# Optimization experiments

Measured on AMD Instinct MI355X. Metric: run time of the kernel, lower is better.

Reference implementation:

```python
import jax, jax.numpy as jnp
import numpy as np

# Hyperparameters (from init_kwargs)
D_MODEL = 1024
D_STATE = 64
HEADDIM = 64
MIMO_RANK = 2
CHUNK = 128
EXPAND = 2
D_INNER = EXPAND * D_MODEL            # 2048
NHEADS = D_INNER // HEADDIM           # 32
G = MIMO_RANK * D_STATE               # effective state channels per head = 128
D_CONV = 4
D_XBC = D_INNER + 2 * NHEADS * G      # conv channels
D_IN_PROJ = 2 * D_INNER + 2 * NHEADS * G + NHEADS  # [z, x, B, C, dt]


def rmsnorm(x, w, eps=1e-5):
    return x * w * jax.lax.rsqrt(jnp.mean(x * x, axis=-1, keepdims=True) + eps)


def setup_inputs() -> dict:
    key = jax.random.key(0)
    ks = jax.random.split(key, 8)
    B, L = 2, 2048
    x = jax.random.normal(ks[0], (B, L, D_MODEL), jnp.float32)
    norm_w = jnp.ones((D_MODEL,), jnp.float32)
    in_proj_w = jax.random.normal(ks[1], (D_IN_PROJ, D_MODEL), jnp.float32) * 0.02
    conv_w = jax.random.normal(ks[2], (D_XBC, D_CONV), jnp.float32) * 0.2
    conv_b = jnp.zeros((D_XBC,), jnp.float32)
    dt_bias = jax.random.uniform(ks[3], (NHEADS,), jnp.float32, minval=-4.0, maxval=-1.0)
    A_log = jnp.log(jax.random.uniform(ks[4], (NHEADS,), jnp.float32, minval=1.0, maxval=8.0))
    D_skip = jnp.ones((NHEADS,), jnp.float32)
    gnorm_w = jnp.ones((D_INNER,), jnp.float32)
    out_proj_w = jax.random.normal(ks[5], (D_MODEL, D_INNER), jnp.float32) * 0.02
    return dict(x=x, norm_w=norm_w, in_proj_w=in_proj_w, conv_w=conv_w, conv_b=conv_b,
                dt_bias=dt_bias, A_log=A_log, D_skip=D_skip, gnorm_w=gnorm_w,
                out_proj_w=out_proj_w)


def _mamba3(u, in_proj_w, conv_w, conv_b, dt_bias, A_log, D_skip, gnorm_w, out_proj_w):
    B, L, _ = u.shape
    H, P = NHEADS, HEADDIM
    nc = L // CHUNK

    zxbcdt = u @ in_proj_w.T                                   # (B,L,D_IN_PROJ)
    z, xbc, dt_raw = jnp.split(zxbcdt, [D_INNER, D_INNER + D_XBC], axis=-1)

    # causal depthwise conv (width D_CONV) + SiLU on [x, B, C]
    xp = jnp.pad(xbc, ((0, 0), (D_CONV - 1, 0), (0, 0)))
    conv = conv_b + sum(xp[:, k:k + L, :] * conv_w[:, k] for k in range(D_CONV))
    xbc = jax.nn.silu(conv)
    xh, Bm, Cm = jnp.split(xbc, [D_INNER, D_INNER + H * G], axis=-1)

    Xc = xh.reshape(B, nc, CHUNK, H, P)
    Bc = Bm.reshape(B, nc, CHUNK, H, G)
    Cc = Cm.reshape(B, nc, CHUNK, H, G)

    dt = jax.nn.softplus(dt_raw + dt_bias)                     # (B,L,H), positive
    A = -jnp.exp(A_log)                                        # (H,), negative
    dtc = dt.reshape(B, nc, CHUNK, H)
    a = dtc * A                                                # log decay, (B,nc,cs,H)
    cum = jnp.cumsum(a, axis=2)                                # inclusive cumsum within chunk

    # intra-chunk (quadratic, causal) part
    cumT = cum.transpose(0, 1, 3, 2)                           # (B,nc,H,cs)
    diff = cumT[..., :, None] - cumT[..., None, :]             # cum_l - cum_s
    mask = jnp.tril(jnp.ones((CHUNK, CHUNK), bool))
    decay = jnp.where(mask, jnp.exp(jnp.where(mask, diff, 0.0)), 0.0)
    dtT = dtc.transpose(0, 1, 3, 2)                            # (B,nc,H,cs)
    scores = jnp.einsum('bclhg,bcshg->bchls', Cc, Bc) * decay * dtT[:, :, :, None, :]
    Y_intra = jnp.einsum('bchls,bcshp->bclhp', scores, Xc)

    # inter-chunk state recurrence
    w = jnp.exp(cum[:, :, -1:, :] - cum) * dtc                 # (B,nc,cs,H)
    S = jnp.einsum('bcshg,bcshp->bchgp', Bc * w[..., None], Xc)  # chunk states
    dlast = jnp.exp(cum[:, :, -1, :])                          # (B,nc,H) total chunk decay

    def step(carry, inp):
        dl, s = inp
        return dl[:, :, None, None] * carry + s, carry

    init = jnp.zeros((B, H, G, P), u.dtype)
    _, Hprev = jax.lax.scan(step, init, (dlast.transpose(1, 0, 2), S.transpose(1, 0, 2, 3, 4)))
    Hprev = Hprev.transpose(1, 0, 2, 3, 4)                     # (B,nc,H,G,P) state before chunk
    Y_inter = jnp.einsum('bclhg,bchgp->bclhp', Cc * jnp.exp(cum)[..., None], Hprev)

    y = (Y_intra + Y_inter + D_skip[:, None] * Xc).reshape(B, L, D_INNER)
    y = rmsnorm(y * jax.nn.silu(z), gnorm_w)                   # gated RMSNorm
    return y @ out_proj_w.T


def reference(x, norm_w, in_proj_w, conv_w, conv_b, dt_bias, A_log, D_skip, gnorm_w, out_proj_w):
    # pre-norm residual wrapper
    return x + _mamba3(rmsnorm(x, norm_w), in_proj_w, conv_w, conv_b,
                       dt_bias, A_log, D_skip, gnorm_w, out_proj_w)
```

## Files before the change

### kernel.cpp

```cpp
#include <hip/hip_runtime.h>

typedef unsigned short u16;
typedef __attribute__((ext_vector_type(8))) short bf16x8;
typedef __attribute__((ext_vector_type(4))) float f32x4;

#define MFMA16(a,b,c) __builtin_amdgcn_mfma_f32_16x16x32_bf16(a,b,c,0,0,0)

#define DMODEL   1024
#define DINNER   2048
#define NHEADS   32
#define HEADDIM  64
#define GDIM     128
#define DXBC     10240
#define DPROJ    12320
#define CHUNK_L  128
#define NCHUNK   16
#define NROWS    4096

__device__ __forceinline__ float b2f(u16 u){ return __uint_as_float(((unsigned)u)<<16); }
__device__ __forceinline__ u16 f2b(float f){
  unsigned u = __float_as_uint(f);
  u += 0x7fffu + ((u>>16)&1u);
  return (u16)(u>>16);
}

__device__ __forceinline__ void gload_lds16(const void* g, void* l){
  __builtin_amdgcn_global_load_lds(
      (const __attribute__((address_space(1))) unsigned int*)g,
      (__attribute__((address_space(3))) unsigned int*)l, 16, 0, 0);
}

__global__ void k_f32_to_bf16(const float* __restrict__ src, u16* __restrict__ dst, int n){
  int i = blockIdx.x*blockDim.x + threadIdx.x;
  int stride = gridDim.x*blockDim.x;
  int n4 = n >> 2;
  for (int j=i; j<n4; j+=stride){
    float4 v = reinterpret_cast<const float4*>(src)[j];
    uint2 o;
    o.x = (unsigned)f2b(v.x) | ((unsigned)f2b(v.y)<<16);
    o.y = (unsigned)f2b(v.z) | ((unsigned)f2b(v.w)<<16);
    reinterpret_cast<uint2*>(dst)[j] = o;
  }
}

__global__ __launch_bounds__(256) void k_rmsnorm_in(const float* __restrict__ x,
                                                    const float* __restrict__ w,
                                                    u16* __restrict__ u){
  int row = blockIdx.x, tid = threadIdx.x;
  float4 v = reinterpret_cast<const float4*>(x + (size_t)row*DMODEL)[tid];
  float ss = v.x*v.x + v.y*v.y + v.z*v.z + v.w*v.w;
  #pragma unroll
  for (int off=32; off>0; off>>=1) ss += __shfl_down(ss, off, 64);
  __shared__ float red[4];
  if ((tid&63)==0) red[tid>>6] = ss;
  __syncthreads();
  float tot = red[0]+red[1]+red[2]+red[3];
  float sc = rsqrtf(tot/(float)DMODEL + 1e-5f);
  float4 wv = reinterpret_cast<const float4*>(w)[tid];
  uint2 o;
  o.x = (unsigned)f2b(v.x*wv.x*sc) | ((unsigned)f2b(v.y*wv.y*sc)<<16);
  o.y = (unsigned)f2b(v.z*wv.z*sc) | ((unsigned)f2b(v.w*wv.w*sc)<<16);
  reinterpret_cast<uint2*>(u + (size_t)row*DMODEL)[tid] = o;
}

__global__ __launch_bounds__(512) void k_gemm1_8ph(const u16* __restrict__ A,
                                                   const u16* __restrict__ W,
                                                   u16* __restrict__ zb,
                                                   u16* __restrict__ xbc){
  __shared__ __align__(16) u16 lds[4*16384];
  const int tid  = threadIdx.x;
  const int lane = tid & 63, w = tid >> 6;
  const int wr = w >> 2, wc = w & 3;
  int bid = blockIdx.x;
  int xcd = bid & 7, g = bid >> 3;
  int st  = xcd*6 + (g >> 4);
  int wi  = g & 15;
  int tm  = (st/12)*4 + (wi>>2);
  int tn  = (st%12)*4 + (wi&3);
  const int m0 = tm*256, n0 = tn*256;

  const int srcslot = ((lane&3) ^ ((lane>>3)&3)) * 8;
  const u16* aS0 = A + (size_t)(m0 + w*16 + (lane>>2))*DMODEL + srcslot;
  const u16* aS1 = aS0 + (size_t)128*DMODEL;
  const u16* bS0 = W + (size_t)(n0 + w*16 + (lane>>2))*DMODEL + srcslot;
  const u16* bS1 = bS0 + (size_t)128*DMODEL;
  const int ldsW = (w*16)*32;
  const int rr = lane & 15;
  const int kb = (((lane>>4) ^ ((lane>>1)&3))) * 8;

  f32x4 acc[8][4];
  #pragma unroll
  for (int i=0;i<8;i++)
    #pragma unroll
    for (int j=0;j<4;j++) acc[i][j] = (f32x4){0,0,0,0};

  int stage_off = 0;
  auto STAGE = [&](int slot){
    u16* base = lds + slot*16384;
    gload_lds16(aS0 + stage_off, base + ldsW);
    gload_lds16(aS1 + stage_off, base + 128*32 + ldsW);
    gload_lds16(bS0 + stage_off, base + 8192 + ldsW);
    gload_lds16(bS1 + stage_off, base + 8192 + 128*32 + ldsW);
    stage_off += 32;
  };
  auto KTILE = [&](int kt, bool do_stage){
    int slot = kt & 3;
    if (do_stage) STAGE((kt+3)&3);
    const u16* As = lds + slot*16384;
    const u16* Bs = As + 8192;
    bf16x8 bf[4];
    #pragma unroll
    for (int tj=0;tj<4;tj++)
      bf[tj] = *(const bf16x8*)&Bs[(wc*64 + tj*16 + rr)*32 + kb];
    #pragma unroll
    for (int r=0;r<2;r++){
      bf16x8 af[4];
      #pragma unroll
      for (int ti=0;ti<4;ti++)
        af[ti] = *(const bf16x8*)&As[(wr*128 + r*64 + ti*16 + rr)*32 + kb];
      __builtin_amdgcn_s_setprio(1);
      #pragma unroll
      for (int ti=0;ti<4;ti++)
        #pragma unroll
        for (int tj=0;tj<4;tj++)
          acc[r*4+ti][tj] = MFMA16(af[ti], bf[tj], acc[r*4+ti][tj]);
      __builtin_amdgcn_s_setprio(0);
    }
  };

  STAGE(0); STAGE(1); STAGE(2);
  asm volatile("s_waitcnt vmcnt(8)" ::: "memory");
  __builtin_amdgcn_s_barrier();
  __builtin_amdgcn_sched_barrier(0);

  for (int kt = 0; kt < 29; ++kt){
    KTILE(kt, true);
    asm volatile("s_waitcnt vmcnt(8)" ::: "memory");
    __builtin_amdgcn_s_barrier();
    __builtin_amdgcn_sched_barrier(0);
  }
  KTILE(29, false);
  asm volatile("s_waitcnt vmcnt(4)" ::: "memory");
  __builtin_amdgcn_s_barrier();
  __builtin_amdgcn_sched_barrier(0);
  KTILE(30, false);
  asm volatile("s_waitcnt vmcnt(0)" ::: "memory");
  __builtin_amdgcn_s_barrier();
  __builtin_amdgcn_sched_barrier(0);
  KTILE(31, false);

  const int row0 = m0 + wr*128 + (lane>>4)*4;
  const int colb = wc*64 + (lane&15);
  if (tn >= 8){
    const int cb = n0 - DINNER;
    #pragma unroll
    for (int ti=0;ti<8;ti++)
      #pragma unroll
      for (int tj=0;tj<4;tj++)
        #pragma unroll
        for (int q=0;q<4;q++)
          xbc[(size_t)(row0 + ti*16 + q)*DXBC + cb + colb + tj*16] = f2b(acc[ti][tj][q]);
  } else {
    #pragma unroll
    for (int ti=0;ti<8;ti++)
      #pragma unroll
      for (int tj=0;tj<4;tj++)
        #pragma unroll
        for (int q=0;q<4;q++)
          zb[(size_t)(row0 + ti*16 + q)*DINNER + n0 + colb + tj*16] = f2b(acc[ti][tj][q]);
  }
}

template<int K>
__device__ __forceinline__ void gemm_core(const u16* __restrict__ A, const u16* __restrict__ W,
                                          int m0, int n0, u16* As, u16* Bs, f32x4 acc[4][4]){
  const int tid  = threadIdx.x;
  const int lane = tid & 63, wv = tid >> 6;
  const int wr = wv >> 1, wc = wv & 1;
  const int r4 = lane >> 2, c8 = (lane & 3) * 8;
  const int rr = lane & 15, kb = (lane >> 4) * 8;

  const u16* aS = A + (size_t)(m0 + wv*32 + r4)*K + c8;
  const u16* bS = W + (size_t)(n0 + wv*32 + r4)*K + c8;
  u16* aD = As + (wv*32)*32;
  u16* bD = Bs + (wv*32)*32;

  #pragma unroll
  for (int i=0;i<4;i++)
    #pragma unroll
    for (int j=0;j<4;j++) acc[i][j] = (f32x4){0,0,0,0};

  for (int k0 = 0; k0 < K; k0 += 32){
    gload_lds16(aS + k0,        aD);
    gload_lds16(aS + 16*K + k0, aD + 16*32);
    gload_lds16(bS + k0,        bD);
    gload_lds16(bS + 16*K + k0, bD + 16*32);
    asm volatile("s_waitcnt vmcnt(0)");
    __syncthreads();
    bf16x8 af[4], bw[4];
    #pragma unroll
    for (int t=0;t<4;t++){
      af[t] = *(const bf16x8*)&As[(wr*64 + t*16 + rr)*32 + kb];
      bw[t] = *(const bf16x8*)&Bs[(wc*64 + t*16 + rr)*32 + kb];
    }
    #pragma unroll
    for (int ti=0;ti<4;ti++)
      #pragma unroll
      for (int tj=0;tj<4;tj++)
        acc[ti][tj] = MFMA16(af[ti], bw[tj], acc[ti][tj]);
    __syncthreads();
  }
}

__global__ __launch_bounds__(256) void k_gemm_dt(const u16* __restrict__ A,
                                                 const u16* __restrict__ W,
                                                 float* __restrict__ dtraw){
  const int lane = threadIdx.x & 63, wv = threadIdx.x >> 6;
  const int m0 = blockIdx.x*32;
  const int n0 = DINNER + DXBC;
  const int r  = lane & 15;
  const int kb = (lane>>4)*8;
  const int k0 = wv*256;
  const u16* a0p = A + (size_t)(m0 + r)*DMODEL + k0 + kb;
  const u16* a1p = a0p + 16*DMODEL;
  const u16* b0p = W + (size_t)(n0 + r)*DMODEL + k0 + kb;
  const u16* b1p = b0p + 16*DMODEL;
  f32x4 acc00={0,0,0,0}, acc01={0,0,0,0}, acc10={0,0,0,0}, acc11={0,0,0,0};
  #pragma unroll
  for (int k=0;k<256;k+=32){
    bf16x8 a0 = *(const bf16x8*)(a0p + k);
    bf16x8 a1 = *(const bf16x8*)(a1p + k);
    bf16x8 b0 = *(const bf16x8*)(b0p + k);
    bf16x8 b1 = *(const bf16x8*)(b1p + k);
    acc00 = MFMA16(a0,b0,acc00);
    acc01 = MFMA16(a0,b1,acc01);
    acc10 = MFMA16(a1,b0,acc10);
    acc11 = MFMA16(a1,b1,acc11);
  }
  __shared__ float part[4][1024];
  int rowb = (lane>>4)*4, col = lane&15;
  #pragma unroll
  for (int rr=0; rr<4; rr++){
    part[wv][(rowb+rr)*32 + col]         = acc00[rr];
    part[wv][(rowb+rr)*32 + col+16]      = acc01[rr];
    part[wv][(rowb+16+rr)*32 + col]      = acc10[rr];
    part[wv][(rowb+16+rr)*32 + col+16]   = acc11[rr];
  }
  __syncthreads();
  int idx = threadIdx.x*4;
  #pragma unroll
  for (int q=0;q<4;q++){
    int i = idx+q;
    dtraw[(size_t)m0*NHEADS + i] = part[0][i]+part[1][i]+part[2][i]+part[3][i];
  }
}

__global__ __launch_bounds__(256) void k_conv(const u16* __restrict__ xbc,
                                              const float* __restrict__ cw,
                                              const float* __restrict__ cb,
                                              u16* __restrict__ xh,
                                              u16* __restrict__ Bm,
                                              u16* __restrict__ Cm){
  int c  = (blockIdx.x*256 + threadIdx.x)*2;
  int row0 = blockIdx.y*8;
  int l0 = row0 & 2047;
  float4 wa = reinterpret_cast<const float4*>(cw)[c];
  float4 wb = reinterpret_cast<const float4*>(cw)[c+1];
  float cba = cb[c], cbb = cb[c+1];
  float a3=0,a2=0,a1=0, b3=0,b2=0,b1=0;
  auto loadpair = [&](int rw, float& fa, float& fb){
    unsigned v = *(const unsigned*)&xbc[(size_t)rw*DXBC + c];
    fa = b2f((u16)v); fb = b2f((u16)(v>>16));
  };
  if (l0 >= 3){
    loadpair(row0-3, a3,b3); loadpair(row0-2, a2,b2); loadpair(row0-1, a1,b1);
  }
  #pragma unroll
  for (int i=0;i<8;i++){
    float a0,b0; loadpair(row0+i, a0,b0);
    float sa = cba + a3*wa.x + a2*wa.y + a1*wa.z + a0*wa.w;
    float sb = cbb + b3*wb.x + b2*wb.y + b1*wb.z + b0*wb.w;
    sa = sa/(1.f+expf(-sa)); sb = sb/(1.f+expf(-sb));
    unsigned o = (unsigned)f2b(sa) | ((unsigned)f2b(sb)<<16);
    int rw = row0 + i;
    if (c < DINNER)            *(unsigned*)&xh[(size_t)rw*DINNER + c] = o;
    else if (c < DINNER+4096)  *(unsigned*)&Bm[(size_t)rw*4096 + (c-DINNER)] = o;
    else                       *(unsigned*)&Cm[(size_t)rw*4096 + (c-DINNER-4096)] = o;
    a3=a2; a2=a1; a1=a0; b3=b2; b2=b1; b1=b0;
  }
}

__global__ __launch_bounds__(128) void k_dtscan(const float* __restrict__ dtraw,
                                                const float* __restrict__ dt_bias,
                                                const float* __restrict__ A_log,
                                                float* __restrict__ dtT,
                                                float* __restrict__ cumT){
  int blk = blockIdx.x;
  int h   = blk & 31;
  int bc  = blk >> 5;
  int s   = threadIdx.x;
  int row = bc*128 + s;
  float xv = dtraw[(size_t)row*NHEADS + h] + dt_bias[h];
  float dt = (xv > 20.f) ? xv : log1pf(expf(xv));
  float a  = dt * (-expf(A_log[h]));
  __shared__ float lds[128];
  lds[s] = a; __syncthreads();
  #pragma unroll
  for (int off=1; off<128; off<<=1){
    float t = (s>=off) ? lds[s-off] : 0.f;
    __syncthreads();
    lds[s] += t;
    __syncthreads();
  }
  dtT[(size_t)blk*128 + s]  = dt;
  cumT[(size_t)blk*128 + s] = lds[s];
}

__global__ __launch_bounds__(256) void k_states(const u16* __restrict__ Bm,
                                                const u16* __restrict__ xh,
                                                const float* __restrict__ dtT,
                                                const float* __restrict__ cumT,
                                                float* __restrict__ S){
  int blk = blockIdx.x;
  int h = blk & 31, bc = blk >> 5;
  __shared__ __align__(16) u16 Bw[128][136];
  __shared__ __align__(16) u16 XT[64][136];
  __shared__ float cum[128], dtv[128];
  int tid = threadIdx.x;
  if (tid < 128){ cum[tid] = cumT[(size_t)blk*128+tid]; dtv[tid] = dtT[(size_t)blk*128+tid]; }
  __syncthreads();
  float clast = cum[127];
  for (int i = tid; i < 128*128; i += 256){
    int s = i >> 7, g = i & 127;
    float w = expf(clast - cum[s]) * dtv[s];
    Bw[g][s] = f2b(b2f(Bm[(size_t)(bc*128+s)*4096 + h*128 + g]) * w);
  }
  for (int i = tid; i < 64*128; i += 256){
    int s = i >> 6, p = i & 63;
    XT[p][s] = xh[(size_t)(bc*128+s)*DINNER + h*64 + p];
  }
  __syncthreads();
  int lane = tid & 63, wv = tid >> 6;
  int r = lane & 15, kb = (lane>>4)*8;
  f32x4 acc[2][4];
  #pragma unroll
  for (int i=0;i<2;i++)
    #pragma unroll
    for (int j=0;j<4;j++) acc[i][j] = (f32x4){0,0,0,0};
  #pragma unroll
  for (int k=0;k<128;k+=32){
    bf16x8 a0 = *(const bf16x8*)&Bw[wv*32 + r][k+kb];
    bf16x8 a1 = *(const bf16x8*)&Bw[wv*32 + 16 + r][k+kb];
    #pragma unroll
    for (int tj=0;tj<4;tj++){
      bf16x8 bb = *(const bf16x8*)&XT[tj*16 + r][k+kb];
      acc[0][tj] = MFMA16(a0,bb,acc[0][tj]);
      acc[1][tj] = MFMA16(a1,bb,acc[1][tj]);
    }
  }
  float* Sp = S + (size_t)blk*8192;
  int g0 = wv*32 + (lane>>4)*4, p0 = lane&15;
  #pragma unroll
  for (int ti=0;ti<2;ti++)
    #pragma unroll
    for (int tj=0;tj<4;tj++)
      #pragma unroll
      for (int rr=0;rr<4;rr++)
        Sp[(g0 + ti*16 + rr)*64 + tj*16 + p0] = acc[ti][tj][rr];
}

__global__ __launch_bounds__(256) void k_scan(const float* __restrict__ S,
                                              const float* __restrict__ cumT,
                                              u16* __restrict__ Hp){
  int slice = blockIdx.x & 7;
  int bh = blockIdx.x >> 3;
  int b = bh >> 5, h = bh & 31;
  int e0 = slice*1024 + threadIdx.x*4;
  float4 carry = {0,0,0,0};
  for (int c=0;c<NCHUNK;c++){
    int blk = (b*16+c)*32 + h;
    float dl = expf(cumT[(size_t)blk*128 + 127]);
    float4 s = *(const float4*)&S[(size_t)blk*8192 + e0];
    uint2 o;
    o.x = (unsigned)f2b(carry.x) | ((unsigned)f2b(carry.y)<<16);
    o.y = (unsigned)f2b(carry.z) | ((unsigned)f2b(carry.w)<<16);
    *reinterpret_cast<uint2*>(&Hp[(size_t)blk*8192 + e0]) = o;
    carry.x = dl*carry.x + s.x;
    carry.y = dl*carry.y + s.y;
    carry.z = dl*carry.z + s.z;
    carry.w = dl*carry.w + s.w;
  }
}

__global__ __launch_bounds__(256) void k_intra(const u16* __restrict__ Cm,
                                               const u16* __restrict__ Bm,
                                               const u16* __restrict__ xh,
                                               const u16* __restrict__ Hp,
                                               const float* __restrict__ dtT,
                                               const float* __restrict__ cumT,
                                               const float* __restrict__ Dskip,
                                               u16* __restrict__ yh){
  int blk = blockIdx.x;
  int h = blk & 31, bc = blk >> 5;
  __shared__ __align__(16) u16 Cl[128][136];
  __shared__ __align__(16) u16 Bl[128][136];
  __shared__ __align__(16) u16 XT[64][136];
  __shared__ __align__(16) u16 HT[64][136];
  __shared__ float cum[128], dtv[128];
  int tid = threadIdx.x;
  if (tid < 128){ cum[tid] = cumT[(size_t)blk*128+tid]; dtv[tid] = dtT[(size_t)blk*128+tid]; }
  for (int i = tid; i < 128*128; i += 256){
    int rw = i >> 7, g = i & 127;
    Cl[rw][g] = Cm[(size_t)(bc*128+rw)*4096 + h*128 + g];
    Bl[rw][g] = Bm[(size_t)(bc*128+rw)*4096 + h*128 + g];
  }
  for (int i = tid; i < 64*128; i += 256){
    int s = i >> 6, p = i & 63;
    XT[p][s] = xh[(size_t)(bc*128+s)*DINNER + h*64 + p];
  }
  for (int i = tid; i < 64*128; i += 256){
    int g = i >> 6, p = i & 63;
    HT[p][g] = Hp[(size_t)blk*8192 + g*64 + p];
  }
  __syncthreads();
  int lane = tid & 63, wv = tid >> 6;
  int r = lane & 15, kb = (lane>>4)*8;

  f32x4 p1[2][8];
  #pragma unroll
  for (int i=0;i<2;i++)
    #pragma unroll
    for (int j=0;j<8;j++) p1[i][j] = (f32x4){0,0,0,0};
  #pragma unroll
  for (int k=0;k<128;k+=32){
    bf16x8 a0 = *(const bf16x8*)&Cl[wv*32 + r][k+kb];
    bf16x8 a1 = *(const bf16x8*)&Cl[wv*32 + 16 + r][k+kb];
    #pragma unroll
    for (int tj=0;tj<8;tj++){
      bf16x8 bb = *(const bf16x8*)&Bl[tj*16 + r][k+kb];
      p1[0][tj] = MFMA16(a0,bb,p1[0][tj]);
      p1[1][tj] = MFMA16(a1,bb,p1[1][tj]);
    }
  }
  __syncthreads();
  int row0 = wv*32 + (lane>>4)*4;
  #pragma unroll
  for (int ti=0;ti<2;ti++)
    #pragma unroll
    for (int tj=0;tj<8;tj++)
      #pragma unroll
      for (int rr=0;rr<4;rr++){
        int l = row0 + ti*16 + rr;
        int s = tj*16 + (lane&15);
        float v = p1[ti][tj][rr];
        v = (s <= l) ? v * expf(cum[l]-cum[s]) * dtv[s] : 0.f;
        Bl[l][s] = f2b(v);
      }
  __syncthreads();

  f32x4 y[2][4];
  #pragma unroll
  for (int i=0;i<2;i++)
    #pragma unroll
    for (int j=0;j<4;j++) y[i][j] = (f32x4){0,0,0,0};
  #pragma unroll
  for (int k=0;k<128;k+=32){
    bf16x8 a0 = *(const bf16x8*)&Cl[wv*32 + r][k+kb];
    bf16x8 a1 = *(const bf16x8*)&Cl[wv*32 + 16 + r][k+kb];
    #pragma unroll
    for (int tj=0;tj<4;tj++){
      bf16x8 bb = *(const bf16x8*)&HT[tj*16 + r][k+kb];
      y[0][tj] = MFMA16(a0,bb,y[0][tj]);
      y[1][tj] = MFMA16(a1,bb,y[1][tj]);
    }
  }
  #pragma unroll
  for (int ti=0;ti<2;ti++){
    #pragma unroll
    for (int rr=0;rr<4;rr++){
      float e = expf(cum[row0 + ti*16 + rr]);
      #pragma unroll
      for (int tj=0;tj<4;tj++) y[ti][tj][rr] *= e;
    }
  }
  #pragma unroll
  for (int k=0;k<128;k+=32){
    bf16x8 a0 = *(const bf16x8*)&Bl[wv*32 + r][k+kb];
    bf16x8 a1 = *(const bf16x8*)&Bl[wv*32 + 16 + r][k+kb];
    #pragma unroll
    for (int tj=0;tj<4;tj++){
      bf16x8 bb = *(const bf16x8*)&XT[tj*16 + r][k+kb];
      y[0][tj] = MFMA16(a0,bb,y[0][tj]);
      y[1][tj] = MFMA16(a1,bb,y[1][tj]);
    }
  }
  float Dh = Dskip[h];
  #pragma unroll
  for (int ti=0;ti<2;ti++)
    #pragma unroll
    for (int tj=0;tj<4;tj++)
      #pragma unroll
      for (int rr=0;rr<4;rr++){
        int l = row0 + ti*16 + rr;
        int p = tj*16 + (lane&15);
        float xv = b2f(XT[p][l]);
        yh[(size_t)(bc*128 + l)*DINNER + h*64 + p] = f2b(y[ti][tj][rr] + Dh*xv);
      }
}

__global__ __launch_bounds__(256) void k_gate(const u16* __restrict__ yh,
                                              const u16* __restrict__ zb,
                                              const float* __restrict__ gw,
                                              u16* __restrict__ out){
  int row = blockIdx.x, tid = threadIdx.x;
  const uint4 yv = reinterpret_cast<const uint4*>(yh + (size_t)row*DINNER)[tid];
  const uint4 zv = reinterpret_cast<const uint4*>(zb + (size_t)row*DINNER)[tid];
  const unsigned* yp = (const unsigned*)&yv;
  const unsigned* zp = (const unsigned*)&zv;
  float t[8]; float ss = 0.f;
  #pragma unroll
  for (int i=0;i<4;i++){
    float y0 = b2f((u16)yp[i]), y1 = b2f((u16)(yp[i]>>16));
    float z0 = b2f((u16)zp[i]), z1 = b2f((u16)(zp[i]>>16));
    float v0 = y0 * (z0 / (1.f + expf(-z0)));
    float v1 = y1 * (z1 / (1.f + expf(-z1)));
    t[2*i] = v0; t[2*i+1] = v1; ss += v0*v0 + v1*v1;
  }
  #pragma unroll
  for (int off=32; off>0; off>>=1) ss += __shfl_down(ss, off, 64);
  __shared__ float red[4];
  if ((tid&63)==0) red[tid>>6] = ss;
  __syncthreads();
  float tot = red[0]+red[1]+red[2]+red[3];
  float g = rsqrtf(tot/(float)DINNER + 1e-5f);
  const float4 g0 = reinterpret_cast<const float4*>(gw)[tid*2];
  const float4 g1 = reinterpret_cast<const float4*>(gw)[tid*2+1];
  uint4 o;
  unsigned* op = (unsigned*)&o;
  float gg[8] = {g0.x,g0.y,g0.z,g0.w,g1.x,g1.y,g1.z,g1.w};
  #pragma unroll
  for (int i=0;i<4;i++)
    op[i] = (unsigned)f2b(t[2*i]*gg[2*i]*g) | ((unsigned)f2b(t[2*i+1]*gg[2*i+1]*g)<<16);
  reinterpret_cast<uint4*>(out + (size_t)row*DINNER)[tid] = o;
}

__global__ __launch_bounds__(256) void k_gemm2(const u16* __restrict__ A,
                                               const u16* __restrict__ W,
                                               const float* __restrict__ xres,
                                               float* __restrict__ out){
  __shared__ __align__(16) u16 As[128*32];
  __shared__ __align__(16) u16 Bs[128*32];
  const int NWG = 8*32, Q = NWG/8;
  int swz = (blockIdx.x & 7)*Q + (blockIdx.x >> 3);
  int tm = swz / 8, tn = swz % 8;
  int m0 = tm*128, n0 = tn*128;
  f32x4 acc[4][4];
  gemm_core<DINNER>(A, W, m0, n0, As, Bs, acc);

  const int lane = threadIdx.x & 63, wv = threadIdx.x >> 6;
  const int wr = wv >> 1, wc = wv & 1;
  int row0 = m0 + wr*64 + (lane>>4)*4;
  int col0 = n0 + wc*64 + (lane&15);
  #pragma unroll
  for (int ti=0;ti<4;ti++)
    #pragma unroll
    for (int tj=0;tj<4;tj++)
      #pragma unroll
      for (int q=0;q<4;q++){
        size_t idx = (size_t)(row0+ti*16+q)*DMODEL + col0 + tj*16;
        out[idx] = acc[ti][tj][q] + xres[idx];
      }
}

extern "C" void kernel_launch(void* const* d_in, const int* in_sizes, int n_in,
                              void* d_out, int out_size, void* d_ws, size_t ws_size,
                              hipStream_t stream) {
  (void)in_sizes; (void)n_in; (void)out_size; (void)ws_size;
  const float* x         = (const float*)d_in[0];
  const float* norm_w    = (const float*)d_in[1];
  const float* in_proj_w = (const float*)d_in[2];
  const float* conv_w    = (const float*)d_in[3];
  const float* conv_b    = (const float*)d_in[4];
  const float* dt_bias   = (const float*)d_in[5];
  const float* A_log     = (const float*)d_in[6];
  const float* D_skip    = (const float*)d_in[7];
  const float* gnorm_w   = (const float*)d_in[8];
  const float* out_proj_w= (const float*)d_in[9];
  float* out = (float*)d_out;

  char* ws = (char*)d_ws;
  size_t off = 0;
  auto alloc = [&](size_t bytes)->char*{
    char* p = ws + off; off = (off + bytes + 255) & ~(size_t)255; return p;
  };
  u16*   W2    = (u16*)  alloc((size_t)DMODEL*DINNER*2);
  u16*   zb    = (u16*)  alloc((size_t)NROWS*DINNER*2);
  float* dtraw = (float*)alloc((size_t)NROWS*NHEADS*4);
  float* dtT   = (float*)alloc((size_t)1024*128*4);
  float* cumT  = (float*)alloc((size_t)1024*128*4);
  u16*   xhb   = (u16*)  alloc((size_t)NROWS*DINNER*2);
  u16*   Bmb   = (u16*)  alloc((size_t)NROWS*4096*2);
  u16*   Cmb   = (u16*)  alloc((size_t)NROWS*4096*2);
  char*  R1    = alloc((size_t)NROWS*DXBC*2);
  u16*   xbcr  = (u16*)R1;
  float* S     = (float*)R1;
  u16*   Hp    = (u16*)(R1 + (size_t)1024*8192*4);
  u16*   yh    = (u16*)R1;
  char*  R2    = alloc((size_t)DPROJ*DMODEL*2 + (size_t)NROWS*DMODEL*2);
  u16*   W1    = (u16*)R2;
  u16*   u_bf  = (u16*)(R2 + (size_t)DPROJ*DMODEL*2);
  u16*   gated = (u16*)R2;

  k_f32_to_bf16<<<2048,256,0,stream>>>(in_proj_w, W1, DPROJ*DMODEL);
  k_f32_to_bf16<<<512,256,0,stream>>>(out_proj_w, W2, DMODEL*DINNER);
  k_rmsnorm_in<<<NROWS,256,0,stream>>>(x, norm_w, u_bf);
  k_gemm1_8ph<<<768,512,0,stream>>>(u_bf, W1, zb, xbcr);
  k_gemm_dt<<<NROWS/32,256,0,stream>>>(u_bf, W1, dtraw);
  k_conv<<<dim3(DXBC/512, NROWS/8),256,0,stream>>>(xbcr, conv_w, conv_b, xhb, Bmb, Cmb);
  k_dtscan<<<1024,128,0,stream>>>(dtraw, dt_bias, A_log, dtT, cumT);
  k_states<<<1024,256,0,stream>>>(Bmb, xhb, dtT, cumT, S);
  k_scan<<<512,256,0,stream>>>(S, cumT, Hp);
  k_intra<<<1024,256,0,stream>>>(Cmb, Bmb, xhb, Hp, dtT, cumT, D_skip, yh);
  k_gate<<<NROWS,256,0,stream>>>(yh, zb, gnorm_w, gated);
  k_gemm2<<<8*32,256,0,stream>>>(gated, W2, x, out);
}
```

Measured before the change: 333.0 us.

## Double-buffer gemm1 with mid-tile staging and pipeline gemm2 with swizzled LDS

```diff
diff --git a/kernel.cpp b/kernel.cpp
--- a/kernel.cpp
+++ b/kernel.cpp
@@ -63,11 +63,11 @@
   reinterpret_cast<uint2*>(u + (size_t)row*DMODEL)[tid] = o;
 }
 
-__global__ __launch_bounds__(512) void k_gemm1_8ph(const u16* __restrict__ A,
-                                                   const u16* __restrict__ W,
-                                                   u16* __restrict__ zb,
-                                                   u16* __restrict__ xbc){
-  __shared__ __align__(16) u16 lds[4*16384];
+__global__ __launch_bounds__(512) void k_gemm1_p2(const u16* __restrict__ A,
+                                                  const u16* __restrict__ W,
+                                                  u16* __restrict__ zb,
+                                                  u16* __restrict__ xbc){
+  __shared__ __align__(16) u16 lds[2*16384];
   const int tid  = threadIdx.x;
   const int lane = tid & 63, w = tid >> 6;
   const int wr = w >> 2, wc = w & 3;
@@ -95,59 +95,63 @@
     for (int j=0;j<4;j++) acc[i][j] = (f32x4){0,0,0,0};
 
   int stage_off = 0;
-  auto STAGE = [&](int slot){
-    u16* base = lds + slot*16384;
+  auto STAGE = [&](int kt){
+    u16* base = lds + (kt&1)*16384;
     gload_lds16(aS0 + stage_off, base + ldsW);
     gload_lds16(aS1 + stage_off, base + 128*32 + ldsW);
     gload_lds16(bS0 + stage_off, base + 8192 + ldsW);
     gload_lds16(bS1 + stage_off, base + 8192 + 128*32 + ldsW);
     stage_off += 32;
   };
-  auto KTILE = [&](int kt, bool do_stage){
-    int slot = kt & 3;
-    if (do_stage) STAGE((kt+3)&3);
-    const u16* As = lds + slot*16384;
+
+  auto KTILE = [&](int kt, int stage_kt){
+    const u16* As = lds + (kt&1)*16384;
     const u16* Bs = As + 8192;
-    bf16x8 bf[4];
+    bf16x8 bf[4], af0[4], af1[4];
     #pragma unroll
     for (int tj=0;tj<4;tj++)
       bf[tj] = *(const bf16x8*)&Bs[(wc*64 + tj*16 + rr)*32 + kb];
     #pragma unroll
-    for (int r=0;r<2;r++){
-      bf16x8 af[4];
-      #pragma unroll
-      for (int ti=0;ti<4;ti++)
-        af[ti] = *(const bf16x8*)&As[(wr*128 + r*64 + ti*16 + rr)*32 + kb];
-      __builtin_amdgcn_s_setprio(1);
-      #pragma unroll
-      for (int ti=0;ti<4;ti++)
-        #pragma unroll
-        for (int tj=0;tj<4;tj++)
-          acc[r*4+ti][tj] = MFMA16(af[ti], bf[tj], acc[r*4+ti][tj]);
-      __builtin_amdgcn_s_setprio(0);
-    }
+    for (int ti=0;ti<4;ti++)
+      af0[ti] = *(const bf16x8*)&As[(wr*128 + ti*16 + rr)*32 + kb];
+    __builtin_amdgcn_s_setprio(1);
+    #pragma unroll
+    for (int ti=0;ti<4;ti++)
+      #pragma unroll
+      for (int tj=0;tj<4;tj++)
+        acc[ti][tj] = MFMA16(af0[ti], bf[tj], acc[ti][tj]);
+    __builtin_amdgcn_s_setprio(0);
+    #pragma unroll
+    for (int ti=0;ti<4;ti++)
+      af1[ti] = *(const bf16x8*)&As[(wr*128 + 64 + ti*16 + rr)*32 + kb];
+    asm volatile("s_waitcnt lgkmcnt(0)" ::: "memory");
+    __builtin_amdgcn_s_barrier();
+    if (stage_kt >= 0) STAGE(stage_kt);
+    __builtin_amdgcn_s_setprio(1);
+    #pragma unroll
+    for (int ti=0;ti<4;ti++)
+      #pragma unroll
+      for (int tj=0;tj<4;tj++)
+        acc[4+ti][tj] = MFMA16(af1[ti], bf[tj], acc[4+ti][tj]);
+    __builtin_amdgcn_s_setprio(0);
   };
 
-  STAGE(0); STAGE(1); STAGE(2);
-  asm volatile("s_waitcnt vmcnt(8)" ::: "memory");
-  __builtin_amdgcn_s_barrier();
-  __builtin_amdgcn_sched_barrier(0);
-
-  for (int kt = 0; kt < 29; ++kt){
-    KTILE(kt, true);
-    asm volatile("s_waitcnt vmcnt(8)" ::: "memory");
-    __builtin_amdgcn_s_barrier();
-    __builtin_amdgcn_sched_barrier(0);
-  }
-  KTILE(29, false);
+  STAGE(0); STAGE(1);
   asm volatile("s_waitcnt vmcnt(4)" ::: "memory");
   __builtin_amdgcn_s_barrier();
   __builtin_amdgcn_sched_barrier(0);
-  KTILE(30, false);
+
+  for (int kt = 0; kt < 30; ++kt){
+    KTILE(kt, kt+2);
+    asm volatile("s_waitcnt vmcnt(4)" ::: "memory");
+    __builtin_amdgcn_s_barrier();
+    __builtin_amdgcn_sched_barrier(0);
+  }
+  KTILE(30, -1);
   asm volatile("s_waitcnt vmcnt(0)" ::: "memory");
   __builtin_amdgcn_s_barrier();
   __builtin_amdgcn_sched_barrier(0);
-  KTILE(31, false);
+  KTILE(31, -1);
 
   const int row0 = m0 + wr*128 + (lane>>4)*4;
   const int colb = wc*64 + (lane&15);
@@ -168,47 +172,6 @@
         #pragma unroll
         for (int q=0;q<4;q++)
           zb[(size_t)(row0 + ti*16 + q)*DINNER + n0 + colb + tj*16] = f2b(acc[ti][tj][q]);
-  }
-}
-
-template<int K>
-__device__ __forceinline__ void gemm_core(const u16* __restrict__ A, const u16* __restrict__ W,
-                                          int m0, int n0, u16* As, u16* Bs, f32x4 acc[4][4]){
-  const int tid  = threadIdx.x;
-  const int lane = tid & 63, wv = tid >> 6;
-  const int wr = wv >> 1, wc = wv & 1;
-  const int r4 = lane >> 2, c8 = (lane & 3) * 8;
-  const int rr = lane & 15, kb = (lane >> 4) * 8;
-
-  const u16* aS = A + (size_t)(m0 + wv*32 + r4)*K + c8;
-  const u16* bS = W + (size_t)(n0 + wv*32 + r4)*K + c8;
-  u16* aD = As + (wv*32)*32;
-  u16* bD = Bs + (wv*32)*32;
-
-  #pragma unroll
-  for (int i=0;i<4;i++)
-    #pragma unroll
-    for (int j=0;j<4;j++) acc[i][j] = (f32x4){0,0,0,0};
-
-  for (int k0 = 0; k0 < K; k0 += 32){
-    gload_lds16(aS + k0,        aD);
-    gload_lds16(aS + 16*K + k0, aD + 16*32);
-    gload_lds16(bS + k0,        bD);
-    gload_lds16(bS + 16*K + k0, bD + 16*32);
-    asm volatile("s_waitcnt vmcnt(0)");
-    __syncthreads();
-    bf16x8 af[4], bw[4];
-    #pragma unroll
-    for (int t=0;t<4;t++){
-      af[t] = *(const bf16x8*)&As[(wr*64 + t*16 + rr)*32 + kb];
-      bw[t] = *(const bf16x8*)&Bs[(wc*64 + t*16 + rr)*32 + kb];
-    }
-    #pragma unroll
-    for (int ti=0;ti<4;ti++)
-      #pragma unroll
-      for (int tj=0;tj<4;tj++)
-        acc[ti][tj] = MFMA16(af[ti], bw[tj], acc[ti][tj]);
-    __syncthreads();
   }
 }
 
@@ -544,21 +507,82 @@
   reinterpret_cast<uint4*>(out + (size_t)row*DINNER)[tid] = o;
 }
 
-__global__ __launch_bounds__(256) void k_gemm2(const u16* __restrict__ A,
-                                               const u16* __restrict__ W,
-                                               const float* __restrict__ xres,
-                                               float* __restrict__ out){
-  __shared__ __align__(16) u16 As[128*32];
-  __shared__ __align__(16) u16 Bs[128*32];
+__global__ __launch_bounds__(256) void k_gemm2_db(const u16* __restrict__ A,
+                                                  const u16* __restrict__ W,
+                                                  const float* __restrict__ xres,
+                                                  float* __restrict__ out){
+  __shared__ __align__(16) u16 lds[2*8192];
+  const int tid  = threadIdx.x;
+  const int lane = tid & 63, wv = tid >> 6;
+  const int wr = wv >> 1, wc = wv & 1;
   const int NWG = 8*32, Q = NWG/8;
   int swz = (blockIdx.x & 7)*Q + (blockIdx.x >> 3);
   int tm = swz / 8, tn = swz % 8;
   int m0 = tm*128, n0 = tn*128;
+
+  const int K = DINNER;
+  const int srcslot = ((lane&3) ^ ((lane>>3)&3)) * 8;
+  const u16* aS0 = A + (size_t)(m0 + wv*32 + (lane>>2))*K + srcslot;
+  const u16* aS1 = aS0 + (size_t)16*K;
+  const u16* bS0 = W + (size_t)(n0 + wv*32 + (lane>>2))*K + srcslot;
+  const u16* bS1 = bS0 + (size_t)16*K;
+  const int ldsW = (wv*32)*32;
+  const int rr = lane & 15;
+  const int kb = (((lane>>4) ^ ((lane>>1)&3))) * 8;
+
   f32x4 acc[4][4];
-  gemm_core<DINNER>(A, W, m0, n0, As, Bs, acc);
-
-  const int lane = threadIdx.x & 63, wv = threadIdx.x >> 6;
-  const int wr = wv >> 1, wc = wv & 1;
+  #pragma unroll
+  for (int i=0;i<4;i++)
+    #pragma unroll
+    for (int j=0;j<4;j++) acc[i][j] = (f32x4){0,0,0,0};
+
+  int stage_off = 0;
+  auto STAGE = [&](int ks){
+    u16* base = lds + (ks&1)*8192;
+    gload_lds16(aS0 + stage_off, base + ldsW);
+    gload_lds16(aS1 + stage_off, base + 16*32 + ldsW);
+    gload_lds16(bS0 + stage_off, base + 4096 + ldsW);
+    gload_lds16(bS1 + stage_off, base + 4096 + 16*32 + ldsW);
+    stage_off += 32;
+  };
+  auto KSTEP = [&](int ks, int stage_ks){
+    const u16* As = lds + (ks&1)*8192;
+    const u16* Bs = As + 4096;
+    bf16x8 af[4], bw[4];
+    #pragma unroll
+    for (int t=0;t<4;t++){
+      af[t] = *(const bf16x8*)&As[(wr*64 + t*16 + rr)*32 + kb];
+      bw[t] = *(const bf16x8*)&Bs[(wc*64 + t*16 + rr)*32 + kb];
+    }
+    asm volatile("s_waitcnt lgkmcnt(0)" ::: "memory");
+    __builtin_amdgcn_s_barrier();
+    if (stage_ks >= 0) STAGE(stage_ks);
+    __builtin_amdgcn_s_setprio(1);
+    #pragma unroll
+    for (int ti=0;ti<4;ti++)
+      #pragma unroll
+      for (int tj=0;tj<4;tj++)
+        acc[ti][tj] = MFMA16(af[ti], bw[tj], acc[ti][tj]);
+    __builtin_amdgcn_s_setprio(0);
+  };
+
+  STAGE(0); STAGE(1);
+  asm volatile("s_waitcnt vmcnt(4)" ::: "memory");
+  __builtin_amdgcn_s_barrier();
+  __builtin_amdgcn_sched_barrier(0);
+  const int NK = K/32;
+  for (int ks = 0; ks < NK-2; ++ks){
+    KSTEP(ks, ks+2);
+    asm volatile("s_waitcnt vmcnt(4)" ::: "memory");
+    __builtin_amdgcn_s_barrier();
+    __builtin_amdgcn_sched_barrier(0);
+  }
+  KSTEP(NK-2, -1);
+  asm volatile("s_waitcnt vmcnt(0)" ::: "memory");
+  __builtin_amdgcn_s_barrier();
+  __builtin_amdgcn_sched_barrier(0);
+  KSTEP(NK-1, -1);
+
   int row0 = m0 + wr*64 + (lane>>4)*4;
   int col0 = n0 + wc*64 + (lane&15);
   #pragma unroll
@@ -614,7 +638,7 @@
   k_f32_to_bf16<<<2048,256,0,stream>>>(in_proj_w, W1, DPROJ*DMODEL);
   k_f32_to_bf16<<<512,256,0,stream>>>(out_proj_w, W2, DMODEL*DINNER);
   k_rmsnorm_in<<<NROWS,256,0,stream>>>(x, norm_w, u_bf);
-  k_gemm1_8ph<<<768,512,0,stream>>>(u_bf, W1, zb, xbcr);
+  k_gemm1_p2<<<768,512,0,stream>>>(u_bf, W1, zb, xbcr);
   k_gemm_dt<<<NROWS/32,256,0,stream>>>(u_bf, W1, dtraw);
   k_conv<<<dim3(DXBC/512, NROWS/8),256,0,stream>>>(xbcr, conv_w, conv_b, xhb, Bmb, Cmb);
   k_dtscan<<<1024,128,0,stream>>>(dtraw, dt_bias, A_log, dtT, cumT);
@@ -622,5 +646,5 @@
   k_scan<<<512,256,0,stream>>>(S, cumT, Hp);
   k_intra<<<1024,256,0,stream>>>(Cmb, Bmb, xhb, Hp, dtT, cumT, D_skip, yh);
   k_gate<<<NROWS,256,0,stream>>>(yh, zb, gnorm_w, gated);
-  k_gemm2<<<8*32,256,0,stream>>>(gated, W2, x, out);
-}
+  k_gemm2_db<<<8*32,256,0,stream>>>(gated, W2, x, out);
+}
```

Result: faster. 325.5 us (-2.3%).
